# Performance work log

Hardware: AMD Instinct MI355X
Metric: run time of the kernel (lower is better)

Reference implementation:

```python
import jax, jax.numpy as jnp
import numpy as np

DIM = 256
HEADS = 8
WS = 7          # window_size
WN = 8          # window_num per side
H = W = WS * WN # 56
B = 32
MLP_HIDDEN = 4 * DIM
SCALE = (DIM // HEADS) ** -0.5
LN_EPS = 1e-5


def _rel_index(ws):
    # pairwise relative position index inside a ws x ws window (dense 0..(2ws-1)^2-1,
    # so remap_position_index is the identity relabeling)
    ch, cw = np.meshgrid(np.arange(ws), np.arange(ws), indexing='ij')
    cf = np.stack([ch.ravel(), cw.ravel()])            # (2, ws*ws)
    rel = cf[:, :, None] - cf[:, None, :]              # (2, N, N)
    rel = rel.transpose(1, 2, 0).astype(np.int32)
    rel[..., 0] += ws - 1
    rel[..., 1] += ws - 1
    rel[..., 0] *= 2 * ws - 1
    return rel.sum(-1)                                 # (N, N) in [0, (2ws-1)^2)


def _layernorm(x, g, b):
    m = x.mean(-1, keepdims=True)
    v = ((x - m) ** 2).mean(-1, keepdims=True)
    return (x - m) * jax.lax.rsqrt(v + LN_EPS) * g + b


def _mhsa(x, qkv_w, qkv_b, proj_w, proj_b, bias):
    # x: (B_, N, C); bias: (nH, N, N) or None
    B_, N, C = x.shape
    hd = C // HEADS
    qkv = (x @ qkv_w.T + qkv_b).reshape(B_, N, 3, HEADS, hd).transpose(2, 0, 3, 1, 4)
    q, k, v = qkv[0], qkv[1], qkv[2]
    attn = jnp.einsum('bhqd,bhkd->bhqk', q * SCALE, k)
    if bias is not None:
        attn = attn + bias[None]
    attn = jax.nn.softmax(attn, axis=-1)
    out = jnp.einsum('bhqk,bhkd->bhqd', attn, v).transpose(0, 2, 1, 3).reshape(B_, N, C)
    return out @ proj_w.T + proj_b


def setup_inputs() -> dict:
    key = jax.random.key(0)
    ks = jax.random.split(key, 8)
    f32 = jnp.float32
    return {
        'regional_tokens': jax.random.normal(ks[0], (B, WN * WN, DIM), f32),
        'x': jax.random.normal(ks[1], (B, H * W, DIM), f32),
        'norm1_g': jnp.ones((DIM,), f32), 'norm1_b': jnp.zeros((DIM,), f32),
        'norm2_g': jnp.ones((DIM,), f32), 'norm2_b': jnp.zeros((DIM,), f32),
        'norm3_g': jnp.ones((DIM,), f32), 'norm3_b': jnp.zeros((DIM,), f32),
        'qkv_w': jax.random.normal(ks[2], (3 * DIM, DIM), f32) * 0.02,
        'qkv_b': jnp.zeros((3 * DIM,), f32),
        'proj_w': jax.random.normal(ks[3], (DIM, DIM), f32) * 0.02,
        'proj_b': jnp.zeros((DIM,), f32),
        'bias_table': jax.random.normal(ks[4], ((2 * WS - 1) ** 2, HEADS), f32) * 0.02,
        'fc1_w': jax.random.normal(ks[5], (MLP_HIDDEN, DIM), f32) * 0.02,
        'fc1_b': jnp.zeros((MLP_HIDDEN,), f32),
        'fc2_w': jax.random.normal(ks[6], (DIM, MLP_HIDDEN), f32) * 0.02,
        'fc2_b': jnp.zeros((DIM,), f32),
        'rel_index': jnp.asarray(_rel_index(WS)),
    }


def reference(regional_tokens, x, norm1_g, norm1_b, norm2_g, norm2_b, norm3_g, norm3_b,
              qkv_w, qkv_b, proj_w, proj_b, bias_table, fc1_w, fc1_b, fc2_w, fc2_b,
              rel_index):
    Bb, L, C = x.shape
    nW = regional_tokens.shape[1]
    ws2 = WS * WS
    # --- RSA: attention over regional tokens (no relative bias) ---
    regional_tokens = regional_tokens + _mhsa(
        _layernorm(regional_tokens, norm1_g, norm1_b), qkv_w, qkv_b, proj_w, proj_b, None)
    # --- window partition of x: (B,H,W,C) -> (nW*B, ws*ws, C) (batch-major) ---
    xw = x.reshape(Bb, H // WS, WS, W // WS, WS, C)
    xw = xw.transpose(0, 1, 3, 2, 4, 5).reshape(-1, ws2, C)
    # regional tokens reshaped window-major, exactly as the torch code does
    reg = regional_tokens.transpose(1, 0, 2).reshape(nW * Bb, 1, C)
    t = jnp.concatenate([reg, xw], axis=1)  # (nW*B, 1+ws2, C)
    # --- LSA relative position bias, zero-padded for the regional token ---
    bias = bias_table[rel_index]                       # (ws2, ws2, nH)
    bias = jnp.pad(bias, ((1, 0), (1, 0), (0, 0)))      # (1+ws2, 1+ws2, nH)
    bias = bias.transpose(2, 0, 1)                      # (nH, N, N)
    t = t + _mhsa(_layernorm(t, norm2_g, norm2_b), qkv_w, qkv_b, proj_w, proj_b, bias)
    # --- MLP ---
    h = _layernorm(t, norm3_g, norm3_b)
    h = jax.nn.gelu(h @ fc1_w.T + fc1_b, approximate=False) @ fc2_w.T + fc2_b
    t = t + h
    # --- split back ---
    reg_out = t[:, 0, :].reshape(nW, Bb, C).transpose(1, 0, 2)   # (B, nW, C)
    xw = t[:, 1:, :].reshape(Bb, H // WS, W // WS, WS, WS, C)
    x_out = xw.transpose(0, 1, 3, 2, 4, 5).reshape(Bb, L, C)
    return reg_out, x_out
```

## Files before the change

### kernel.cpp

```cpp
#include <hip/hip_runtime.h>
#include <math.h>

#define SCALE_Q 0.17677669529663687f

typedef __attribute__((ext_vector_type(8))) short bf16x8;
typedef __attribute__((ext_vector_type(4))) float f32x4;
typedef __attribute__((ext_vector_type(4))) unsigned short u16x4;

static __device__ __forceinline__ unsigned short f2bf(float f) {
    unsigned int u = __float_as_uint(f);
    u += 0x7FFF + ((u >> 16) & 1);
    return (unsigned short)(u >> 16);
}

static __device__ __forceinline__ float gelu_fast(float v) {
    float s = v * (0.7978845608f + 0.0356774081f * v * v);
    float e = __expf(-2.0f * s);
    return v * __builtin_amdgcn_rcpf(1.0f + e);
}

__global__ void prep_kernel(const float* __restrict__ qkv_w, const float* __restrict__ proj_w,
                            const float* __restrict__ fc1_w, const float* __restrict__ fc2_w,
                            const float* __restrict__ bias_table, const int* __restrict__ rel_index,
                            unsigned short* __restrict__ wq, unsigned short* __restrict__ wp,
                            unsigned short* __restrict__ w1, unsigned short* __restrict__ w2,
                            float* __restrict__ bias_pad) {
    int tid = blockIdx.x * blockDim.x + threadIdx.x;
    int stride = gridDim.x * blockDim.x;
    for (int i = tid; i < 768 * 256; i += stride) wq[i] = f2bf(qkv_w[i]);
    for (int i = tid; i < 256 * 256; i += stride) wp[i] = f2bf(proj_w[i]);
    for (int i = tid; i < 1024 * 256; i += stride) w1[i] = f2bf(fc1_w[i]);
    for (int i = tid; i < 256 * 1024; i += stride) w2[i] = f2bf(fc2_w[i]);
    for (int i = tid; i < 8 * 64 * 64; i += stride) {
        int h = i >> 12, q = (i >> 6) & 63, k = i & 63;
        float v;
        if (k >= 50) v = -1e30f;
        else if (q == 0 || k == 0 || q >= 50) v = 0.f;
        else v = bias_table[rel_index[(q - 1) * 49 + (k - 1)] * 8 + h];
        bias_pad[i] = v;
    }
}

template <int IS_RSA>
__global__ __launch_bounds__(1024, 4) void attn_kernel(
    const float* __restrict__ reg_tok, const float* __restrict__ x,
    const float* __restrict__ reg2_in, float* __restrict__ out,
    const float* __restrict__ ln_g, const float* __restrict__ ln_b,
    const unsigned short* __restrict__ wq, const float* __restrict__ qkv_b,
    const unsigned short* __restrict__ wp, const float* __restrict__ proj_b,
    const float* __restrict__ bias_pad) {
    __shared__ __align__(16) unsigned char smem[140288];
    unsigned short* regA = (unsigned short*)smem;
    unsigned short* regB = (unsigned short*)(smem + 36864);
    unsigned short* vT   = (unsigned short*)(smem + 103424);

    const int tid = threadIdx.x;
    const int lane = tid & 63;
    const int wid = tid >> 6;
    const int l15 = lane & 15;
    const int lg = lane >> 4;
    const int u = blockIdx.x;
    const int NV = IS_RSA ? 64 : 50;
    const f32x4 fzero = {0.f, 0.f, 0.f, 0.f};

    int reg_off = 0, xb = 0, wi = 0, wj = 0;
    if (!IS_RSA) {
        reg_off = ((u & 31) * 64 + (u >> 5)) * 256;
        xb = u >> 6;
        int xn = u & 63;
        wi = xn >> 3; wj = xn & 7;
    }

    for (int r = wid; r < 64; r += 16) {
        if (r < NV) {
            const float* src;
            if (IS_RSA) src = reg_tok + (u * 64 + r) * 256;
            else if (r == 0) src = reg2_in + reg_off;
            else {
                int p = r - 1;
                src = x + (xb * 3136 + (wi * 7 + p / 7) * 56 + (wj * 7 + p % 7)) * 256;
            }
            f32x4 v = *(const f32x4*)(src + lane * 4);
            float s = v[0] + v[1] + v[2] + v[3];
            float s2 = v[0] * v[0] + v[1] * v[1] + v[2] * v[2] + v[3] * v[3];
            #pragma unroll
            for (int m = 1; m < 64; m <<= 1) { s += __shfl_xor(s, m); s2 += __shfl_xor(s2, m); }
            float mean = s * 0.00390625f;
            float rstd = rsqrtf(s2 * 0.00390625f - mean * mean + 1e-5f);
            u16x4 o;
            #pragma unroll
            for (int j = 0; j < 4; ++j) {
                int c = lane * 4 + j;
                o[j] = f2bf((v[j] - mean) * rstd * ln_g[c] + ln_b[c]);
            }
            *(u16x4*)(regA + r * 264 + lane * 4) = o;
        } else {
            u16x4 z = {0, 0, 0, 0};
            *(u16x4*)(regA + r * 264 + lane * 4) = z;
        }
    }
    __syncthreads();

    const int h = wid >> 1;
    const int qb = (wid & 1) * 32;

    {
        f32x4 acc[4][3];
        #pragma unroll
        for (int mi = 0; mi < 4; ++mi)
            #pragma unroll
            for (int t = 0; t < 3; ++t) acc[mi][t] = fzero;
        #pragma unroll
        for (int ks = 0; ks < 8; ++ks) {
            int k = ks * 32 + lg * 8;
            bf16x8 a[4], b[3];
            #pragma unroll
            for (int mi = 0; mi < 4; ++mi) a[mi] = *(const bf16x8*)(regA + (mi * 16 + l15) * 264 + k);
            #pragma unroll
            for (int t = 0; t < 3; ++t) b[t] = *(const bf16x8*)(wq + (wid * 48 + t * 16 + l15) * 256 + k);
            #pragma unroll
            for (int mi = 0; mi < 4; ++mi)
                #pragma unroll
                for (int t = 0; t < 3; ++t)
                    acc[mi][t] = __builtin_amdgcn_mfma_f32_16x16x32_bf16(a[mi], b[t], acc[mi][t], 0, 0, 0);
        }
        #pragma unroll
        for (int mi = 0; mi < 4; ++mi)
            #pragma unroll
            for (int t = 0; t < 3; ++t) {
                int col = wid * 48 + t * 16 + l15;
                float bias = qkv_b[col];
                #pragma unroll
                for (int r = 0; r < 4; ++r) {
                    int row = mi * 16 + lg * 4 + r;
                    unsigned short hv = f2bf(acc[mi][t][r] + bias);
                    if (col < 512) regB[row * 520 + col] = hv;
                    else vT[(col - 512) * 72 + row] = hv;
                }
            }
    }

    f32x4 bv[4][2];
    if (!IS_RSA) {
        #pragma unroll
        for (int mi = 0; mi < 4; ++mi)
            #pragma unroll
            for (int nj = 0; nj < 2; ++nj)
                bv[mi][nj] = *(const f32x4*)(bias_pad + h * 4096 + (qb + nj * 16 + l15) * 64 + mi * 16 + lg * 4);
    }
    __syncthreads();

    f32x4 st[4][2];
    {
        int k0 = h * 32 + lg * 8;
        bf16x8 af[4], bfq[2];
        #pragma unroll
        for (int mi = 0; mi < 4; ++mi) af[mi] = *(const bf16x8*)(regB + (mi * 16 + l15) * 520 + 256 + k0);
        #pragma unroll
        for (int nj = 0; nj < 2; ++nj) bfq[nj] = *(const bf16x8*)(regB + (qb + nj * 16 + l15) * 520 + k0);
        #pragma unroll
        for (int mi = 0; mi < 4; ++mi)
            #pragma unroll
            for (int nj = 0; nj < 2; ++nj)
                st[mi][nj] = __builtin_amdgcn_mfma_f32_16x16x32_bf16(af[mi], bfq[nj], fzero, 0, 0, 0);
    }

    u16x4 pf[4][2];
    #pragma unroll
    for (int nj = 0; nj < 2; ++nj) {
        float ps[4][4];
        float mx = -3.0e38f;
        #pragma unroll
        for (int mi = 0; mi < 4; ++mi)
            #pragma unroll
            for (int r = 0; r < 4; ++r) {
                float t = st[mi][nj][r] * SCALE_Q;
                if (!IS_RSA) t += bv[mi][nj][r];
                ps[mi][r] = t;
                mx = fmaxf(mx, t);
            }
        mx = fmaxf(mx, __shfl_xor(mx, 16));
        mx = fmaxf(mx, __shfl_xor(mx, 32));
        float sum = 0.f;
        #pragma unroll
        for (int mi = 0; mi < 4; ++mi)
            #pragma unroll
            for (int r = 0; r < 4; ++r) { ps[mi][r] = __expf(ps[mi][r] - mx); sum += ps[mi][r]; }
        sum += __shfl_xor(sum, 16);
        sum += __shfl_xor(sum, 32);
        float inv = __builtin_amdgcn_rcpf(sum);
        #pragma unroll
        for (int mi = 0; mi < 4; ++mi) {
            u16x4 p4;
            #pragma unroll
            for (int r = 0; r < 4; ++r) p4[r] = f2bf(ps[mi][r] * inv);
            pf[mi][nj] = p4;
        }
    }

    f32x4 ov[2][2];
    #pragma unroll
    for (int m2 = 0; m2 < 2; ++m2) { ov[m2][0] = fzero; ov[m2][1] = fzero; }
    #pragma unroll
    for (int kt = 0; kt < 4; ++kt) {
        bf16x8 pb[2];
        #pragma unroll
        for (int nj = 0; nj < 2; ++nj) {
            bf16x8 t;
            t[0] = (short)pf[kt][nj][0]; t[1] = (short)pf[kt][nj][1];
            t[2] = (short)pf[kt][nj][2]; t[3] = (short)pf[kt][nj][3];
            t[4] = 0; t[5] = 0; t[6] = 0; t[7] = 0;
            pb[nj] = t;
        }
        #pragma unroll
        for (int m2 = 0; m2 < 2; ++m2) {
            u16x4 av = *(const u16x4*)(vT + (h * 32 + m2 * 16 + l15) * 72 + kt * 16 + lg * 4);
            bf16x8 a8;
            a8[0] = (short)av[0]; a8[1] = (short)av[1]; a8[2] = (short)av[2]; a8[3] = (short)av[3];
            a8[4] = 0; a8[5] = 0; a8[6] = 0; a8[7] = 0;
            #pragma unroll
            for (int nj = 0; nj < 2; ++nj)
                ov[m2][nj] = __builtin_amdgcn_mfma_f32_16x16x32_bf16(a8, pb[nj], ov[m2][nj], 0, 0, 0);
        }
    }
    #pragma unroll
    for (int m2 = 0; m2 < 2; ++m2)
        #pragma unroll
        for (int nj = 0; nj < 2; ++nj) {
            u16x4 o4;
            #pragma unroll
            for (int r = 0; r < 4; ++r) o4[r] = f2bf(ov[m2][nj][r]);
            *(u16x4*)(regA + (qb + nj * 16 + l15) * 264 + h * 32 + m2 * 16 + lg * 4) = o4;
        }
    __syncthreads();

    {
        int nb = wid * 16;
        f32x4 acc[4];
        #pragma unroll
        for (int mi = 0; mi < 4; ++mi) acc[mi] = fzero;
        #pragma unroll
        for (int ks = 0; ks < 8; ++ks) {
            int k = ks * 32 + lg * 8;
            bf16x8 a[4], b;
            #pragma unroll
            for (int mi = 0; mi < 4; ++mi) a[mi] = *(const bf16x8*)(regA + (mi * 16 + l15) * 264 + k);
            b = *(const bf16x8*)(wp + (nb + l15) * 256 + k);
            #pragma unroll
            for (int mi = 0; mi < 4; ++mi)
                acc[mi] = __builtin_amdgcn_mfma_f32_16x16x32_bf16(a[mi], b, acc[mi], 0, 0, 0);
        }
        int col = nb + l15;
        float pb = proj_b[col];
        #pragma unroll
        for (int mi = 0; mi < 4; ++mi)
            #pragma unroll
            for (int r = 0; r < 4; ++r) {
                int row = mi * 16 + lg * 4 + r;
                if (row < NV) {
                    float val = acc[mi][r] + pb;
                    if (IS_RSA) {
                        int off = (u * 64 + row) * 256 + col;
                        out[off] = val + reg_tok[off];
                    } else if (row == 0) {
                        out[reg_off + col] = val + reg2_in[reg_off + col];
                    } else {
                        int p = row - 1;
                        int off = (xb * 3136 + (wi * 7 + p / 7) * 56 + (wj * 7 + p % 7)) * 256 + col;
                        out[524288 + off] = val + x[off];
                    }
                }
            }
    }
}

__global__ __launch_bounds__(512, 2) void mlp_kernel(
    float* __restrict__ dout,
    const float* __restrict__ ln_g, const float* __restrict__ ln_b,
    const unsigned short* __restrict__ w1, const float* __restrict__ b1,
    const unsigned short* __restrict__ w2, const float* __restrict__ b2) {
    __shared__ __align__(16) unsigned short xst[64 * 264];
    __shared__ __align__(16) unsigned short hld[2][64 * 136];
    const int tid = threadIdx.x;
    const int lane = tid & 63;
    const int wid = tid >> 6;
    const int l15 = lane & 15;
    const int lg = lane >> 4;
    const int row0 = blockIdx.x * 64;
    const f32x4 fzero = {0.f, 0.f, 0.f, 0.f};

    #pragma unroll
    for (int i = 0; i < 8; ++i) {
        int r = wid * 8 + i;
        f32x4 v = *(const f32x4*)(dout + (row0 + r) * 256 + lane * 4);
        float s = v[0] + v[1] + v[2] + v[3];
        float s2 = v[0] * v[0] + v[1] * v[1] + v[2] * v[2] + v[3] * v[3];
        #pragma unroll
        for (int m = 1; m < 64; m <<= 1) { s += __shfl_xor(s, m); s2 += __shfl_xor(s2, m); }
        float mean = s * 0.00390625f;
        float rstd = rsqrtf(s2 * 0.00390625f - mean * mean + 1e-5f);
        u16x4 o;
        #pragma unroll
        for (int j = 0; j < 4; ++j) {
            int c = lane * 4 + j;
            o[j] = f2bf((v[j] - mean) * rstd * ln_g[c] + ln_b[c]);
        }
        *(u16x4*)(xst + r * 264 + lane * 4) = o;
    }
    __syncthreads();

    bf16x8 afr[4][8];
    #pragma unroll
    for (int mi = 0; mi < 4; ++mi)
        #pragma unroll
        for (int ks = 0; ks < 8; ++ks)
            afr[mi][ks] = *(const bf16x8*)(xst + (mi * 16 + l15) * 264 + ks * 32 + lg * 8);

    f32x4 acc2[4][2];
    #pragma unroll
    for (int mi = 0; mi < 4; ++mi) { acc2[mi][0] = fzero; acc2[mi][1] = fzero; }

    for (int c = 0; c < 8; ++c) {
        unsigned short* hb = &hld[c & 1][0];
        f32x4 acc1[4];
        #pragma unroll
        for (int mi = 0; mi < 4; ++mi) acc1[mi] = fzero;
        #pragma unroll
        for (int ks = 0; ks < 8; ++ks) {
            bf16x8 b = *(const bf16x8*)(w1 + (c * 128 + wid * 16 + l15) * 256 + ks * 32 + lg * 8);
            #pragma unroll
            for (int mi = 0; mi < 4; ++mi)
                acc1[mi] = __builtin_amdgcn_mfma_f32_16x16x32_bf16(afr[mi][ks], b, acc1[mi], 0, 0, 0);
        }
        {
            int hc = wid * 16 + l15;
            float bb = b1[c * 128 + hc];
            #pragma unroll
            for (int mi = 0; mi < 4; ++mi)
                #pragma unroll
                for (int r = 0; r < 4; ++r)
                    hb[(mi * 16 + lg * 4 + r) * 136 + hc] = f2bf(gelu_fast(acc1[mi][r] + bb));
        }
        __syncthreads();
        #pragma unroll
        for (int ks = 0; ks < 4; ++ks) {
            int k = ks * 32 + lg * 8;
            bf16x8 a[4], b[2];
            #pragma unroll
            for (int mi = 0; mi < 4; ++mi)
                a[mi] = *(const bf16x8*)(hb + (mi * 16 + l15) * 136 + k);
            #pragma unroll
            for (int ni = 0; ni < 2; ++ni)
                b[ni] = *(const bf16x8*)(w2 + (wid * 32 + ni * 16 + l15) * 1024 + c * 128 + k);
            #pragma unroll
            for (int mi = 0; mi < 4; ++mi)
                #pragma unroll
                for (int ni = 0; ni < 2; ++ni)
                    acc2[mi][ni] = __builtin_amdgcn_mfma_f32_16x16x32_bf16(a[mi], b[ni], acc2[mi][ni], 0, 0, 0);
        }
    }
    #pragma unroll
    for (int mi = 0; mi < 4; ++mi)
        #pragma unroll
        for (int ni = 0; ni < 2; ++ni) {
            int col = wid * 32 + ni * 16 + l15;
            float bb = b2[col];
            #pragma unroll
            for (int r = 0; r < 4; ++r) {
                int row = row0 + mi * 16 + lg * 4 + r;
                float* dst = dout + row * 256 + col;
                *dst = acc2[mi][ni][r] + bb + *dst;
            }
        }
}

extern "C" void kernel_launch(void* const* d_in, const int* in_sizes, int n_in,
                              void* d_out, int out_size, void* d_ws, size_t ws_size,
                              hipStream_t stream) {
    const float* regional = (const float*)d_in[0];
    const float* x = (const float*)d_in[1];
    const float* n1g = (const float*)d_in[2];
    const float* n1b = (const float*)d_in[3];
    const float* n2g = (const float*)d_in[4];
    const float* n2b = (const float*)d_in[5];
    const float* n3g = (const float*)d_in[6];
    const float* n3b = (const float*)d_in[7];
    const float* qkvw = (const float*)d_in[8];
    const float* qkvb = (const float*)d_in[9];
    const float* projw = (const float*)d_in[10];
    const float* projb = (const float*)d_in[11];
    const float* btab = (const float*)d_in[12];
    const float* f1w = (const float*)d_in[13];
    const float* f1b = (const float*)d_in[14];
    const float* f2w = (const float*)d_in[15];
    const float* f2b = (const float*)d_in[16];
    const int* relidx = (const int*)d_in[17];

    unsigned char* ws = (unsigned char*)d_ws;
    unsigned short* wq = (unsigned short*)(ws);
    unsigned short* wp = (unsigned short*)(ws + 393216);
    unsigned short* w1 = (unsigned short*)(ws + 524288);
    unsigned short* w2 = (unsigned short*)(ws + 1048576);
    float* bias_pad    = (float*)(ws + 1572864);
    float* reg2        = (float*)(ws + 1703936);

    float* out = (float*)d_out;

    prep_kernel<<<512, 256, 0, stream>>>(qkvw, projw, f1w, f2w, btab, relidx, wq, wp, w1, w2, bias_pad);
    attn_kernel<1><<<32, 1024, 0, stream>>>(regional, x, nullptr, reg2, n1g, n1b, wq, qkvb, wp, projb, nullptr);
    attn_kernel<0><<<2048, 1024, 0, stream>>>(regional, x, reg2, out, n2g, n2b, wq, qkvb, wp, projb, bias_pad);
    mlp_kernel<<<1600, 512, 0, stream>>>(out, n3g, n3b, w1, f1b, w2, f2b);
}
```

Baseline: 545.9 us.

## Prefetch MLP weight fragments into registers and stream activations from LDS

The MLP kernel stops holding the whole LayerNorm'd activation tile in registers and reads A fragments from shared memory on each k-step. The registers this frees hold fc1 and fc2 weight fragments, which are prefetched one hidden chunk ahead so global weight loads overlap the MFMA work. Launch bounds go from 2 to 4 blocks per SM and the chunk loop is fully unrolled. The aim is to hide global load latency and raise occupancy, at the cost of more LDS read traffic and a risk of register spills under the tighter bound.

```diff
diff --git a/kernel.cpp b/kernel.cpp
--- a/kernel.cpp
+++ b/kernel.cpp
@@ -274,7 +274,7 @@
     }
 }
 
-__global__ __launch_bounds__(512, 2) void mlp_kernel(
+__global__ __launch_bounds__(512, 4) void mlp_kernel(
     float* __restrict__ dout,
     const float* __restrict__ ln_g, const float* __restrict__ ln_b,
     const unsigned short* __restrict__ w1, const float* __restrict__ b1,
@@ -307,19 +307,23 @@
         }
         *(u16x4*)(xst + r * 264 + lane * 4) = o;
     }
+
+    bf16x8 w1f[8], w2f[8];
+    #pragma unroll
+    for (int ks = 0; ks < 8; ++ks)
+        w1f[ks] = *(const bf16x8*)(w1 + (wid * 16 + l15) * 256 + ks * 32 + lg * 8);
+    #pragma unroll
+    for (int ks = 0; ks < 4; ++ks)
+        #pragma unroll
+        for (int ni = 0; ni < 2; ++ni)
+            w2f[ks * 2 + ni] = *(const bf16x8*)(w2 + (wid * 32 + ni * 16 + l15) * 1024 + ks * 32 + lg * 8);
     __syncthreads();
 
-    bf16x8 afr[4][8];
-    #pragma unroll
-    for (int mi = 0; mi < 4; ++mi)
-        #pragma unroll
-        for (int ks = 0; ks < 8; ++ks)
-            afr[mi][ks] = *(const bf16x8*)(xst + (mi * 16 + l15) * 264 + ks * 32 + lg * 8);
-
     f32x4 acc2[4][2];
     #pragma unroll
     for (int mi = 0; mi < 4; ++mi) { acc2[mi][0] = fzero; acc2[mi][1] = fzero; }
 
+    #pragma unroll
     for (int c = 0; c < 8; ++c) {
         unsigned short* hb = &hld[c & 1][0];
         f32x4 acc1[4];
@@ -327,10 +331,19 @@
         for (int mi = 0; mi < 4; ++mi) acc1[mi] = fzero;
         #pragma unroll
         for (int ks = 0; ks < 8; ++ks) {
-            bf16x8 b = *(const bf16x8*)(w1 + (c * 128 + wid * 16 + l15) * 256 + ks * 32 + lg * 8);
-            #pragma unroll
-            for (int mi = 0; mi < 4; ++mi)
-                acc1[mi] = __builtin_amdgcn_mfma_f32_16x16x32_bf16(afr[mi][ks], b, acc1[mi], 0, 0, 0);
+            int k = ks * 32 + lg * 8;
+            bf16x8 a[4];
+            #pragma unroll
+            for (int mi = 0; mi < 4; ++mi)
+                a[mi] = *(const bf16x8*)(xst + (mi * 16 + l15) * 264 + k);
+            #pragma unroll
+            for (int mi = 0; mi < 4; ++mi)
+                acc1[mi] = __builtin_amdgcn_mfma_f32_16x16x32_bf16(a[mi], w1f[ks], acc1[mi], 0, 0, 0);
+        }
+        if (c < 7) {
+            #pragma unroll
+            for (int ks = 0; ks < 8; ++ks)
+                w1f[ks] = *(const bf16x8*)(w1 + ((c + 1) * 128 + wid * 16 + l15) * 256 + ks * 32 + lg * 8);
         }
         {
             int hc = wid * 16 + l15;
@@ -345,18 +358,22 @@
         #pragma unroll
         for (int ks = 0; ks < 4; ++ks) {
             int k = ks * 32 + lg * 8;
-            bf16x8 a[4], b[2];
+            bf16x8 a[4];
             #pragma unroll
             for (int mi = 0; mi < 4; ++mi)
                 a[mi] = *(const bf16x8*)(hb + (mi * 16 + l15) * 136 + k);
-            #pragma unroll
-            for (int ni = 0; ni < 2; ++ni)
-                b[ni] = *(const bf16x8*)(w2 + (wid * 32 + ni * 16 + l15) * 1024 + c * 128 + k);
             #pragma unroll
             for (int mi = 0; mi < 4; ++mi)
                 #pragma unroll
                 for (int ni = 0; ni < 2; ++ni)
-                    acc2[mi][ni] = __builtin_amdgcn_mfma_f32_16x16x32_bf16(a[mi], b[ni], acc2[mi][ni], 0, 0, 0);
+                    acc2[mi][ni] = __builtin_amdgcn_mfma_f32_16x16x32_bf16(a[mi], w2f[ks * 2 + ni], acc2[mi][ni], 0, 0, 0);
+        }
+        if (c < 7) {
+            #pragma unroll
+            for (int ks = 0; ks < 4; ++ks)
+                #pragma unroll
+                for (int ni = 0; ni < 2; ++ni)
+                    w2f[ks * 2 + ni] = *(const bf16x8*)(w2 + (wid * 32 + ni * 16 + l15) * 1024 + (c + 1) * 128 + ks * 32 + lg * 8);
         }
     }
     #pragma unroll
```

New measurement: 485.4 us (median of 4 runs). 11.1% less time.
